# Optimization experiments

Measured on AMD Instinct MI355X. Metric: run time of the kernel, lower is better.

Reference implementation:

```python
import jax, jax.numpy as jnp
from jax import lax
import numpy as np

B, C, HH, WW = 8, 64, 128, 128
N = HH * WW
EPS = 1e-5


def _roll_h(xn, sign):
    # per-channel cyclic roll along H: out[b,c,h,w] = xn[b,c,(h - sign*c) % H, w]
    _, Cx, Hx, _ = xn.shape
    c = jnp.arange(Cx)[:, None]
    idx = (jnp.arange(Hx)[None, :] - sign * jnp.arange(Cx)[:, None]) % Hx  # (C,H)
    return xn[:, c, idx, :]


def _roll_w(xn, sign):
    return _roll_h(xn.transpose(0, 1, 3, 2), sign).transpose(0, 1, 3, 2)


def _ch_linear(xn, w, b):
    # nn.Linear over the channel dim of a BCHW tensor (token-MLP on (B,N,C))
    return jnp.einsum('bchw,cd->bdhw', xn, w) + b[None, :, None, None]


def _bn(xn, g, b):
    # BatchNorm2d, training-mode stats (biased var over B,H,W)
    m = xn.mean(axis=(0, 2, 3), keepdims=True)
    v = xn.var(axis=(0, 2, 3), keepdims=True)
    return (xn - m) * lax.rsqrt(v + EPS) * g[None, :, None, None] + b[None, :, None, None]


def _dwconv(xn, w, dil, pad):
    return lax.conv_general_dilated(xn, w, (1, 1), ((pad, pad), (pad, pad)),
                                    rhs_dilation=(dil, dil),
                                    dimension_numbers=('NCHW', 'OIHW', 'NCHW'),
                                    feature_group_count=xn.shape[1])


def _pc(xn, w):
    # 1x1 pointwise conv, no bias; w: (C_out, C_in)
    return jnp.einsum('bchw,oc->bohw', xn, w)


def lgff_forward(x, fc1_w, fc1_b, fc2_w, fc2_b, fc3_w, fc3_b, fc4_w, fc4_b,
                 fc5_w, fc5_b, ln_g, ln_b, pc_w, dw_w, dw_b, dw_bn_g, dw_bn_b,
                 dd_w, dd_bn_g, dd_bn_b, se_w1, se_b1, se_w2, se_b2, H, W):
    Bx, Nx, Cx = x.shape
    xn = x.transpose(0, 2, 1).reshape(Bx, Cx, H, W)
    # branch 1: roll+c along H -> fc1 -> GELU -> roll+c along W -> fc2
    a = jax.nn.gelu(_ch_linear(_roll_h(xn, 1), fc1_w, fc1_b), approximate=False)
    x_1 = _ch_linear(_roll_w(a, 1), fc2_w, fc2_b) + xn
    # branch 2: roll-c along W -> fc3 -> GELU -> roll+c along H -> fc4
    b = jax.nn.gelu(_ch_linear(_roll_w(xn, -1), fc3_w, fc3_b), approximate=False)
    x_2 = _ch_linear(_roll_h(b, 1), fc4_w, fc4_b) + xn
    # concat along feature dim (token layout dim=2 == channel dim here), LayerNorm(2C), fc5
    xc = jnp.concatenate([x_1, x_2], axis=1)  # (B, 2C, H, W)
    m = xc.mean(axis=1, keepdims=True)
    v = xc.var(axis=1, keepdims=True)
    xc = (xc - m) * lax.rsqrt(v + EPS) * ln_g[None, :, None, None] + ln_b[None, :, None, None]
    x1 = _ch_linear(xc, fc5_w, fc5_b) + xn
    # conv fusion part
    x2 = _pc(x1, pc_w)
    y = jax.nn.relu(_bn(_dwconv(x2, dw_w, 1, 1) + dw_b[None, :, None, None], dw_bn_g, dw_bn_b))
    y = jax.nn.relu(_bn(_dwconv(y, dd_w, 2, 2), dd_bn_g, dd_bn_b))
    y = _pc(y, pc_w)
    # four branches x3..x6 share identical weights/input -> identical outputs
    x7 = 4.0 * (x2 * y)
    # SE block
    s = x7.mean(axis=(2, 3), keepdims=True)  # (B,C,1,1)
    e = jax.nn.relu(jnp.einsum('bcij,oc->boij', s, se_w1) + se_b1[None, :, None, None])
    e = jax.nn.sigmoid(jnp.einsum('bcij,oc->boij', e, se_w2) + se_b2[None, :, None, None])
    return x7 + x7 * e  # (B, C, H, W)


def setup_inputs():
    key = jax.random.key(0)
    ks = jax.random.split(key, 12)
    r = C // 8
    inp = {
        'x': jax.random.normal(ks[0], (B, N, C), jnp.float32),
        'fc1_w': jax.random.normal(ks[1], (C, C), jnp.float32) * 0.02,
        'fc1_b': jnp.zeros((C,), jnp.float32),
        'fc2_w': jax.random.normal(ks[2], (C, C), jnp.float32) * 0.02,
        'fc2_b': jnp.zeros((C,), jnp.float32),
        'fc3_w': jax.random.normal(ks[3], (C, C), jnp.float32) * 0.02,
        'fc3_b': jnp.zeros((C,), jnp.float32),
        'fc4_w': jax.random.normal(ks[4], (C, C), jnp.float32) * 0.02,
        'fc4_b': jnp.zeros((C,), jnp.float32),
        'fc5_w': jax.random.normal(ks[5], (2 * C, C), jnp.float32) * 0.02,
        'fc5_b': jnp.zeros((C,), jnp.float32),
        'ln_g': jnp.ones((2 * C,), jnp.float32),
        'ln_b': jnp.zeros((2 * C,), jnp.float32),
        'pc_w': jax.random.normal(ks[6], (C, C), jnp.float32) * np.sqrt(2.0 / C).astype(np.float32),
        'dw_w': jax.random.normal(ks[7], (C, 1, 3, 3), jnp.float32) * np.sqrt(2.0 / 9.0).astype(np.float32),
        'dw_b': jnp.zeros((C,), jnp.float32),
        'dw_bn_g': jnp.ones((C,), jnp.float32),
        'dw_bn_b': jnp.zeros((C,), jnp.float32),
        'dd_w': jax.random.normal(ks[8], (C, 1, 3, 3), jnp.float32) * np.sqrt(2.0 / 9.0).astype(np.float32),
        'dd_bn_g': jnp.ones((C,), jnp.float32),
        'dd_bn_b': jnp.zeros((C,), jnp.float32),
        'se_w1': jax.random.normal(ks[9], (r, C), jnp.float32) * np.sqrt(2.0 / r).astype(np.float32),
        'se_b1': jnp.zeros((r,), jnp.float32),
        'se_w2': jax.random.normal(ks[10], (C, r), jnp.float32) * np.sqrt(2.0 / C).astype(np.float32),
        'se_b2': jnp.zeros((C,), jnp.float32),
        'H': HH,
        'W': WW,
    }
    return inp


def reference(x, fc1_w, fc1_b, fc2_w, fc2_b, fc3_w, fc3_b, fc4_w, fc4_b,
              fc5_w, fc5_b, ln_g, ln_b, pc_w, dw_w, dw_b, dw_bn_g, dw_bn_b,
              dd_w, dd_bn_g, dd_bn_b, se_w1, se_b1, se_w2, se_b2, H, W):
    return lgff_forward(x, fc1_w, fc1_b, fc2_w, fc2_b, fc3_w, fc3_b, fc4_w, fc4_b,
                        fc5_w, fc5_b, ln_g, ln_b, pc_w, dw_w, dw_b, dw_bn_g, dw_bn_b,
                        dd_w, dd_bn_g, dd_bn_b, se_w1, se_b1, se_w2, se_b2, H, W)
```

## Files before the change

kernel.cpp:

```cpp
#include <hip/hip_runtime.h>

constexpr int NB  = 8;
constexpr int NC  = 64;
constexpr int NH  = 128;
constexpr int NW  = 128;
constexpr int NHW = NH * NW;
constexpr int CHW = NC * NHW;
constexpr int SZ  = NB * CHW;
constexpr int NPOS = NB * NHW;
constexpr float EPS = 1e-5f;

typedef unsigned short u16;
using bf8   = __attribute__((ext_vector_type(8))) short;
using u16x8 = __attribute__((ext_vector_type(8))) u16;
using f32x4 = __attribute__((ext_vector_type(4))) float;

static __device__ inline short f2bf(float f) {
    union { float f; unsigned int u; } v; v.f = f;
    unsigned int r = v.u + 0x7fffu + ((v.u >> 16) & 1u);
    return (short)(r >> 16);
}
static __device__ inline float bf2f(u16 u) {
    union { unsigned int i; float f; } v; v.i = ((unsigned int)u) << 16;
    return v.f;
}

__global__ void k_transpose(const float* __restrict__ x, u16* __restrict__ xn) {
    __shared__ float t[64 * 65];
    int b   = blockIdx.x >> 8;
    int hw0 = (blockIdx.x & 255) << 6;
    int tid = threadIdx.x;
    #pragma unroll
    for (int k = 0; k < 16; ++k) {
        int idx = tid + (k << 8);
        int c = idx & 63, hwl = idx >> 6;
        t[c * 65 + hwl] = x[((size_t)b * NHW + hw0 + hwl) * NC + c];
    }
    __syncthreads();
    #pragma unroll
    for (int k = 0; k < 16; ++k) {
        int idx = tid + (k << 8);
        int hwl = idx & 63, c = idx >> 6;
        xn[(size_t)(b * NC + c) * NHW + hw0 + hwl] = (u16)f2bf(t[c * 65 + hwl]);
    }
}

__global__ void k_pq(const float* __restrict__ w5, const float* __restrict__ lng,
                     const float* __restrict__ lnb, float* __restrict__ PQ) {
    int d = threadIdx.x;
    float P = 0.f, Q = 0.f;
    for (int c = 0; c < 128; ++c) {
        float wv = w5[c * 64 + d];
        P += lng[c] * wv;
        Q += lnb[c] * wv;
    }
    PQ[d] = P; PQ[64 + d] = Q;
}

__global__ __launch_bounds__(256) void
k_mfc2(const u16* __restrict__ xn,
       const float* __restrict__ w1, const float* __restrict__ b1,
       const float* __restrict__ w3, const float* __restrict__ b3,
       u16* __restrict__ t1, u16* __restrict__ t2) {
    __shared__ short wA[64 * 64];
    __shared__ short wB[64 * 64];
    int tid = threadIdx.x;
    int l = tid & 63, wv = tid >> 6;

    #pragma unroll
    for (int i = 0; i < 8; ++i) {
        int c0 = wv * 2 + i * 8;
        unsigned int pa = (unsigned int)(u16)f2bf(w1[c0 * 64 + l]) |
                          ((unsigned int)(u16)f2bf(w1[(c0 + 1) * 64 + l]) << 16);
        *(unsigned int*)&wA[l * 64 + (c0 ^ ((l & 7) << 3))] = pa;
        unsigned int pb = (unsigned int)(u16)f2bf(w3[c0 * 64 + l]) |
                          ((unsigned int)(u16)f2bf(w3[(c0 + 1) * 64 + l]) << 16);
        *(unsigned int*)&wB[l * 64 + (c0 ^ ((l & 7) << 3))] = pb;
    }
    __syncthreads();

    int q = l >> 4, col = l & 15;
    int p  = blockIdx.x * 64 + wv * 16 + col;
    int b  = p >> 14;
    int hw = p & (NHW - 1);
    int h  = hw >> 7, w = hw & 127;
    const u16* inb = xn + (size_t)b * CHW;

    f32x4 acc1[4], acc2[4];
    #pragma unroll
    for (int dt = 0; dt < 4; ++dt) {
        acc1[dt] = (f32x4){0.f, 0.f, 0.f, 0.f};
        acc2[dt] = (f32x4){0.f, 0.f, 0.f, 0.f};
    }
    #pragma unroll
    for (int ks = 0; ks < 2; ++ks) {
        bf8 f1, f2;
        #pragma unroll
        for (int j = 0; j < 8; ++j) {
            int c = ks * 32 + q * 8 + j;
            f1[j] = (short)inb[c * NHW + (((h - c) & 127) << 7) + w];
            f2[j] = (short)inb[c * NHW + (h << 7) + ((w + c) & 127)];
        }
        #pragma unroll
        for (int dt = 0; dt < 4; ++dt) {
            int d = dt * 16 + col;
            int wo = (ks * 32 + q * 8) ^ ((d & 7) << 3);
            acc1[dt] = __builtin_amdgcn_mfma_f32_16x16x32_bf16(*(bf8*)&wA[d * 64 + wo], f1, acc1[dt], 0, 0, 0);
            acc2[dt] = __builtin_amdgcn_mfma_f32_16x16x32_bf16(*(bf8*)&wB[d * 64 + wo], f2, acc2[dt], 0, 0, 0);
        }
    }

    size_t obase = (size_t)b * CHW + hw;
    #pragma unroll
    for (int dt = 0; dt < 4; ++dt) {
        #pragma unroll
        for (int r = 0; r < 4; ++r) {
            int d = dt * 16 + q * 4 + r;
            float v1 = acc1[dt][r] + b1[d];
            v1 = 0.5f * v1 * (1.f + erff(v1 * 0.70710678118654752f));
            float v2 = acc2[dt][r] + b3[d];
            v2 = 0.5f * v2 * (1.f + erff(v2 * 0.70710678118654752f));
            t1[obase + (size_t)d * NHW] = (u16)f2bf(v1);
            t2[obase + (size_t)d * NHW] = (u16)f2bf(v2);
        }
    }
}

__global__ __launch_bounds__(256) void
k_ffuse(const u16* __restrict__ t1, const u16* __restrict__ t2,
        const u16* __restrict__ xnb,
        const float* __restrict__ fc2w, const float* __restrict__ fc2b,
        const float* __restrict__ fc4w, const float* __restrict__ fc4b,
        const float* __restrict__ w5, const float* __restrict__ lng,
        const float* __restrict__ PQ, const float* __restrict__ b5,
        u16* __restrict__ x1out) {
    __shared__ short wA[64 * 64];
    __shared__ short wB[64 * 64];
    __shared__ short wG[64 * 128];
    __shared__ short xt[64 * 136];

    int tid = threadIdx.x;
    int l = tid & 63, wv = tid >> 6;

    #pragma unroll
    for (int i = 0; i < 8; ++i) {
        int c0 = wv * 2 + i * 8;
        unsigned int pa = (unsigned int)(u16)f2bf(fc2w[c0 * 64 + l]) |
                          ((unsigned int)(u16)f2bf(fc2w[(c0 + 1) * 64 + l]) << 16);
        *(unsigned int*)&wA[l * 64 + (c0 ^ ((l & 7) << 3))] = pa;
        unsigned int pb = (unsigned int)(u16)f2bf(fc4w[c0 * 64 + l]) |
                          ((unsigned int)(u16)f2bf(fc4w[(c0 + 1) * 64 + l]) << 16);
        *(unsigned int*)&wB[l * 64 + (c0 ^ ((l & 7) << 3))] = pb;
    }
    #pragma unroll
    for (int i = 0; i < 16; ++i) {
        int c0 = wv * 2 + i * 8;
        unsigned int pk = (unsigned int)(u16)f2bf(lng[c0] * w5[c0 * 64 + l]) |
                          ((unsigned int)(u16)f2bf(lng[c0 + 1] * w5[(c0 + 1) * 64 + l]) << 16);
        *(unsigned int*)&wG[l * 128 + (c0 ^ ((l & 7) << 3))] = pk;
    }
    __syncthreads();

    int q = l >> 4, col = l & 15;
    int p  = blockIdx.x * 64 + wv * 16 + col;
    int b  = p >> 14;
    int hw = p & (NHW - 1);
    int h  = hw >> 7, w = hw & 127;
    size_t base = (size_t)b * CHW;
    int pos = wv * 16 + col;

    f32x4 acc1[4], acc2[4];
    #pragma unroll
    for (int dt = 0; dt < 4; ++dt) {
        acc1[dt] = (f32x4){0.f, 0.f, 0.f, 0.f};
        acc2[dt] = (f32x4){0.f, 0.f, 0.f, 0.f};
    }
    #pragma unroll
    for (int ks = 0; ks < 2; ++ks) {
        bf8 f1, f2;
        #pragma unroll
        for (int j = 0; j < 8; ++j) {
            int c = ks * 32 + q * 8 + j;
            f1[j] = (short)t1[base + c * NHW + (h << 7) + ((w - c) & 127)];
            f2[j] = (short)t2[base + c * NHW + (((h - c) & 127) << 7) + w];
        }
        #pragma unroll
        for (int dt = 0; dt < 4; ++dt) {
            int d = dt * 16 + col;
            int wo = (ks * 32 + q * 8) ^ ((d & 7) << 3);
            acc1[dt] = __builtin_amdgcn_mfma_f32_16x16x32_bf16(*(bf8*)&wA[d * 64 + wo], f1, acc1[dt], 0, 0, 0);
            acc2[dt] = __builtin_amdgcn_mfma_f32_16x16x32_bf16(*(bf8*)&wB[d * 64 + wo], f2, acc2[dt], 0, 0, 0);
        }
    }

    float xr[16];
    #pragma unroll
    for (int dt = 0; dt < 4; ++dt)
        #pragma unroll
        for (int r = 0; r < 4; ++r)
            xr[dt * 4 + r] = bf2f(xnb[base + (size_t)(dt * 16 + q * 4 + r) * NHW + hw]);

    float s = 0.f, sq = 0.f;
    #pragma unroll
    for (int dt = 0; dt < 4; ++dt) {
        float v1[4], v2[4];
        #pragma unroll
        for (int r = 0; r < 4; ++r) {
            int d = dt * 16 + q * 4 + r;
            v1[r] = acc1[dt][r] + fc2b[d] + xr[dt * 4 + r];
            v2[r] = acc2[dt][r] + fc4b[d] + xr[dt * 4 + r];
            s += v1[r] + v2[r];
            sq += v1[r] * v1[r] + v2[r] * v2[r];
        }
        unsigned int pk0 = (unsigned int)(u16)f2bf(v1[0]) | ((unsigned int)(u16)f2bf(v1[1]) << 16);
        unsigned int pk1 = (unsigned int)(u16)f2bf(v1[2]) | ((unsigned int)(u16)f2bf(v1[3]) << 16);
        *(uint2*)&xt[pos * 136 + dt * 16 + q * 4] = make_uint2(pk0, pk1);
        unsigned int pk2 = (unsigned int)(u16)f2bf(v2[0]) | ((unsigned int)(u16)f2bf(v2[1]) << 16);
        unsigned int pk3 = (unsigned int)(u16)f2bf(v2[2]) | ((unsigned int)(u16)f2bf(v2[3]) << 16);
        *(uint2*)&xt[pos * 136 + 64 + dt * 16 + q * 4] = make_uint2(pk2, pk3);
    }
    s  += __shfl_xor(s, 16);  s += __shfl_xor(s, 32);
    sq += __shfl_xor(sq, 16); sq += __shfl_xor(sq, 32);
    float m    = s * (1.f / 128.f);
    float var  = sq * (1.f / 128.f) - m * m;
    float rstd = rsqrtf(var + EPS);
    float mr   = m * rstd;
    __syncthreads();

    f32x4 acc[4];
    #pragma unroll
    for (int dt = 0; dt < 4; ++dt) acc[dt] = (f32x4){0.f, 0.f, 0.f, 0.f};
    #pragma unroll
    for (int ks = 0; ks < 4; ++ks) {
        bf8 bfr = *(bf8*)&xt[pos * 136 + ks * 32 + q * 8];
        #pragma unroll
        for (int dt = 0; dt < 4; ++dt) {
            int d = dt * 16 + col;
            bf8 afr = *(bf8*)&wG[d * 128 + ((ks * 32 + q * 8) ^ ((d & 7) << 3))];
            acc[dt] = __builtin_amdgcn_mfma_f32_16x16x32_bf16(afr, bfr, acc[dt], 0, 0, 0);
        }
    }

    size_t obase = base + hw;
    #pragma unroll
    for (int dt = 0; dt < 4; ++dt) {
        #pragma unroll
        for (int r = 0; r < 4; ++r) {
            int d = dt * 16 + q * 4 + r;
            float val = rstd * acc[dt][r] + PQ[64 + d] - mr * PQ[d] + b5[d] + xr[dt * 4 + r];
            x1out[obase + (size_t)d * NHW] = (u16)f2bf(val);
        }
    }
}

template<bool BNRELU_IN>
__global__ __launch_bounds__(256) void
k_mfc(const u16* __restrict__ in, const float* __restrict__ wgt,
      const float* __restrict__ meanc, const float* __restrict__ rstdc,
      const float* __restrict__ bng, const float* __restrict__ bnb,
      u16* __restrict__ out) {
    __shared__ short wt[64 * 64];
    __shared__ float scl[64], sft[64];
    int tid = threadIdx.x;
    int l = tid & 63, wv = tid >> 6;

    #pragma unroll
    for (int i = 0; i < 16; ++i) {
        int d = wv * 16 + i;
        wt[d * 64 + (l ^ ((d & 7) << 3))] = f2bf(wgt[d * 64 + l]);
    }
    if (BNRELU_IN && tid < 64) {
        float s = rstdc[tid] * bng[tid];
        scl[tid] = s;
        sft[tid] = bnb[tid] - meanc[tid] * s;
    }
    __syncthreads();

    int q = l >> 4, col = l & 15;
    int p  = blockIdx.x * 64 + wv * 16 + col;
    int b  = p >> 14;
    int hw = p & (NHW - 1);
    const u16* inb = in + (size_t)b * CHW;

    f32x4 acc[4];
    #pragma unroll
    for (int dt = 0; dt < 4; ++dt) acc[dt] = (f32x4){0.f, 0.f, 0.f, 0.f};

    #pragma unroll
    for (int ks = 0; ks < 2; ++ks) {
        bf8 bfr;
        #pragma unroll
        for (int j = 0; j < 8; ++j) {
            int c = ks * 32 + q * 8 + j;
            u16 raw = inb[c * NHW + hw];
            if (BNRELU_IN) {
                float v = fmaxf(bf2f(raw) * scl[c] + sft[c], 0.f);
                bfr[j] = f2bf(v);
            } else {
                bfr[j] = (short)raw;
            }
        }
        #pragma unroll
        for (int dt = 0; dt < 4; ++dt) {
            int d = dt * 16 + col;
            bf8 afr = *(bf8*)&wt[d * 64 + ((ks * 32 + q * 8) ^ ((d & 7) << 3))];
            acc[dt] = __builtin_amdgcn_mfma_f32_16x16x32_bf16(afr, bfr, acc[dt], 0, 0, 0);
        }
    }

    size_t obase = (size_t)b * CHW + hw;
    #pragma unroll
    for (int dt = 0; dt < 4; ++dt)
        #pragma unroll
        for (int r = 0; r < 4; ++r) {
            int d = dt * 16 + q * 4 + r;
            out[obase + (size_t)d * NHW] = (u16)f2bf(acc[dt][r]);
        }
}

template<int DIL, bool HASBIAS, bool BNIN>
__global__ __launch_bounds__(256) void
k_dwlds(const u16* __restrict__ in, const float* __restrict__ wgt,
        const float* __restrict__ bias,
        const float* __restrict__ meanc, const float* __restrict__ rstdc,
        const float* __restrict__ bng, const float* __restrict__ bnb,
        u16* __restrict__ out, float* __restrict__ psum, float* __restrict__ psq) {
    constexpr int STR = 136;
    __shared__ float tile[36 * STR];
    __shared__ float ss[256], sq[256];

    int blk = ((blockIdx.x & 7) << 8) | (blockIdx.x >> 3);
    int q   = blk & 3;
    int bc  = blk >> 2;
    int c   = bc & 63;
    int r0  = q * 32;
    int tid = threadIdx.x;
    const u16* ip = in + (size_t)bc * NHW;

    float scale = 0.f, shift = 0.f;
    if (BNIN) { scale = rstdc[c] * bng[c]; shift = bnb[c] - meanc[c] * scale; }

    #pragma unroll 1
    for (int idx = tid; idx < 36 * 16; idx += 256) {
        int lr = idx >> 4, u = idx & 15;
        int gr = r0 - 2 + lr;
        float v[8] = {0.f, 0.f, 0.f, 0.f, 0.f, 0.f, 0.f, 0.f};
        if (gr >= 0 && gr < NH) {
            u16x8 raw = *(const u16x8*)(ip + gr * NW + u * 8);
            #pragma unroll
            for (int j = 0; j < 8; ++j) {
                float f = bf2f(raw[j]);
                if (BNIN) f = fmaxf(f * scale + shift, 0.f);
                v[j] = f;
            }
        }
        *(float4*)&tile[lr * STR + 4 + u * 8]     = make_float4(v[0], v[1], v[2], v[3]);
        *(float4*)&tile[lr * STR + 4 + u * 8 + 4] = make_float4(v[4], v[5], v[6], v[7]);
        if (u == 0)  *(float4*)&tile[lr * STR]       = make_float4(0.f, 0.f, 0.f, 0.f);
        if (u == 15) *(float4*)&tile[lr * STR + 132] = make_float4(0.f, 0.f, 0.f, 0.f);
    }
    __syncthreads();

    float wc[9];
    #pragma unroll
    for (int k = 0; k < 9; ++k) wc[k] = wgt[c * 9 + k];

    int row  = tid >> 3;
    int col0 = (tid & 7) * 16;
    float o[16];
    float bb = HASBIAS ? bias[c] : 0.f;
    #pragma unroll
    for (int j = 0; j < 16; ++j) o[j] = bb;

    #pragma unroll
    for (int i = 0; i < 3; ++i) {
        const float* rp = &tile[(row + 2 + (i - 1) * DIL) * STR + 4 + col0];
        float4 A  = *(const float4*)(rp - 4);
        float4 B0 = *(const float4*)(rp);
        float4 B1 = *(const float4*)(rp + 4);
        float4 B2 = *(const float4*)(rp + 8);
        float4 B3 = *(const float4*)(rp + 12);
        float4 Cc = *(const float4*)(rp + 16);
        float ww[24] = {A.x,A.y,A.z,A.w, B0.x,B0.y,B0.z,B0.w, B1.x,B1.y,B1.z,B1.w,
                        B2.x,B2.y,B2.z,B2.w, B3.x,B3.y,B3.z,B3.w, Cc.x,Cc.y,Cc.z,Cc.w};
        float w0 = wc[3 * i], w1 = wc[3 * i + 1], w2 = wc[3 * i + 2];
        #pragma unroll
        for (int j = 0; j < 16; ++j)
            o[j] += w0 * ww[4 + j - DIL] + w1 * ww[4 + j] + w2 * ww[4 + j + DIL];
    }

    u16* op = out + (size_t)bc * NHW + (r0 + row) * NW + col0;
    u16x8 o1, o2;
    #pragma unroll
    for (int j = 0; j < 8; ++j) { o1[j] = (u16)f2bf(o[j]); o2[j] = (u16)f2bf(o[8 + j]); }
    *(u16x8*)(op)     = o1;
    *(u16x8*)(op + 8) = o2;

    float s = 0.f, qq = 0.f;
    #pragma unroll
    for (int j = 0; j < 16; ++j) { s += o[j]; qq += o[j] * o[j]; }
    ss[tid] = s; sq[tid] = qq; __syncthreads();
    for (int off = 128; off > 0; off >>= 1) {
        if (tid < off) { ss[tid] += ss[tid + off]; sq[tid] += sq[tid + off]; }
        __syncthreads();
    }
    if (tid == 0) { psum[blk] = ss[0]; psq[blk] = sq[0]; }
}

__global__ void k_bn_finalize(const float* __restrict__ psum, const float* __restrict__ psq,
                              float* __restrict__ meanc, float* __restrict__ rstdc) {
    int c = threadIdx.x;
    float s = 0.f, qv = 0.f;
    for (int b = 0; b < NB; ++b)
        #pragma unroll
        for (int j = 0; j < 4; ++j) {
            int idx = ((b * 64 + c) << 2) + j;
            s += psum[idx]; qv += psq[idx];
        }
    const float inv = 1.f / (float)(NB * NHW);
    float m = s * inv;
    float v = qv * inv - m * m;
    meanc[c] = m;
    rstdc[c] = rsqrtf(v + EPS);
}

__global__ void k_se_reduce(const u16* __restrict__ x2, const u16* __restrict__ y3,
                            float* __restrict__ s4) {
    __shared__ float ss[256];
    int q   = blockIdx.x & 3;
    int bc  = blockIdx.x >> 2;
    int tid = threadIdx.x;
    const u16* a  = x2 + (size_t)bc * NHW + q * (NHW / 4);
    const u16* b_ = y3 + (size_t)bc * NHW + q * (NHW / 4);
    float acc = 0.f;
    #pragma unroll
    for (int i = 0; i < 2; ++i) {
        u16x8 av = *(const u16x8*)(a + (tid + i * 256) * 8);
        u16x8 bv = *(const u16x8*)(b_ + (tid + i * 256) * 8);
        #pragma unroll
        for (int j = 0; j < 8; ++j) acc += bf2f(av[j]) * bf2f(bv[j]);
    }
    ss[tid] = acc; __syncthreads();
    for (int o = 128; o > 0; o >>= 1) {
        if (tid < o) ss[tid] += ss[tid + o];
        __syncthreads();
    }
    if (tid == 0) s4[blockIdx.x] = ss[0];
}

__global__ void k_se_mlp(const float* __restrict__ s4, const float* __restrict__ w1,
                         const float* __restrict__ b1, const float* __restrict__ w2,
                         const float* __restrict__ b2, float* __restrict__ e) {
    __shared__ float sh[64], e1[8];
    int b = blockIdx.x, tid = threadIdx.x;
    float sv = 0.f;
    #pragma unroll
    for (int j = 0; j < 4; ++j) sv += s4[(b * 64 + tid) * 4 + j];
    sh[tid] = sv * (4.f / (float)NHW);
    __syncthreads();
    if (tid < 8) {
        float a = b1[tid];
        for (int c = 0; c < 64; ++c) a += sh[c] * w1[tid * 64 + c];
        e1[tid] = a > 0.f ? a : 0.f;
    }
    __syncthreads();
    float a = b2[tid];
    #pragma unroll
    for (int j = 0; j < 8; ++j) a += e1[j] * w2[tid * 8 + j];
    e[b * 64 + tid] = 1.f / (1.f + expf(-a));
}

__global__ void k_final8(const u16* __restrict__ x2, const u16* __restrict__ y3,
                         const float* __restrict__ e, float* __restrict__ out) {
    int t  = blockIdx.x * 256 + threadIdx.x;
    int bc = t >> 11;
    float f = 4.f * (1.f + e[bc]);
    u16x8 av = *(const u16x8*)(x2 + (size_t)t * 8);
    u16x8 bv = *(const u16x8*)(y3 + (size_t)t * 8);
    float4 o0, o1;
    o0.x = f * bf2f(av[0]) * bf2f(bv[0]); o0.y = f * bf2f(av[1]) * bf2f(bv[1]);
    o0.z = f * bf2f(av[2]) * bf2f(bv[2]); o0.w = f * bf2f(av[3]) * bf2f(bv[3]);
    o1.x = f * bf2f(av[4]) * bf2f(bv[4]); o1.y = f * bf2f(av[5]) * bf2f(bv[5]);
    o1.z = f * bf2f(av[6]) * bf2f(bv[6]); o1.w = f * bf2f(av[7]) * bf2f(bv[7]);
    *(float4*)(out + (size_t)t * 8)     = o0;
    *(float4*)(out + (size_t)t * 8 + 4) = o1;
}

extern "C" void kernel_launch(void* const* d_in, const int* in_sizes, int n_in,
                              void* d_out, int out_size, void* d_ws, size_t ws_size,
                              hipStream_t stream) {
    const float* x     = (const float*)d_in[0];
    const float* fc1w  = (const float*)d_in[1];
    const float* fc1b  = (const float*)d_in[2];
    const float* fc2w  = (const float*)d_in[3];
    const float* fc2b  = (const float*)d_in[4];
    const float* fc3w  = (const float*)d_in[5];
    const float* fc3b  = (const float*)d_in[6];
    const float* fc4w  = (const float*)d_in[7];
    const float* fc4b  = (const float*)d_in[8];
    const float* fc5w  = (const float*)d_in[9];
    const float* fc5b  = (const float*)d_in[10];
    const float* lng   = (const float*)d_in[11];
    const float* lnb   = (const float*)d_in[12];
    const float* pcw   = (const float*)d_in[13];
    const float* dww   = (const float*)d_in[14];
    const float* dwb   = (const float*)d_in[15];
    const float* dwbng = (const float*)d_in[16];
    const float* dwbnb = (const float*)d_in[17];
    const float* ddw   = (const float*)d_in[18];
    const float* ddbng = (const float*)d_in[19];
    const float* ddbnb = (const float*)d_in[20];
    const float* sew1  = (const float*)d_in[21];
    const float* seb1  = (const float*)d_in[22];
    const float* sew2  = (const float*)d_in[23];
    const float* seb2  = (const float*)d_in[24];

    float* out = (float*)d_out;
    u16* wsu = (u16*)d_ws;
    u16* bufA = wsu;
    u16* bufB = wsu + (size_t)SZ;
    u16* bufC = wsu + (size_t)2 * SZ;
    u16* bufD = wsu + (size_t)3 * SZ;
    float* st = (float*)(wsu + (size_t)4 * SZ);
    float* psumA  = st;
    float* psqA   = st + 2048;
    float* meanc1 = st + 4096;
    float* rstdc1 = st + 4160;
    float* meanc2 = st + 4224;
    float* rstdc2 = st + 4288;
    float* svec   = st + 4352;
    float* evec   = st + 6400;
    float* pqv    = st + 6912;

    dim3 blk(256);
    const float* nil = nullptr;

    k_transpose<<<NB * (NHW / 64), blk, 0, stream>>>(x, bufA);
    k_pq<<<1, 64, 0, stream>>>(fc5w, lng, lnb, pqv);
    k_mfc2<<<NPOS / 64, blk, 0, stream>>>(bufA, fc1w, fc1b, fc3w, fc3b, bufB, bufC);
    k_ffuse<<<NPOS / 64, blk, 0, stream>>>(bufB, bufC, bufA, fc2w, fc2b, fc4w, fc4b,
                                           fc5w, lng, pqv, fc5b, bufD);
    k_mfc<false><<<NPOS / 64, blk, 0, stream>>>(bufD, pcw, nil, nil, nil, nil, bufA);
    k_dwlds<1, true, false><<<2048, blk, 0, stream>>>(bufA, dww, dwb, nil, nil, nil, nil, bufB, psumA, psqA);
    k_bn_finalize<<<1, 64, 0, stream>>>(psumA, psqA, meanc1, rstdc1);
    k_dwlds<2, false, true><<<2048, blk, 0, stream>>>(bufB, ddw, nil, meanc1, rstdc1, dwbng, dwbnb, bufC, psumA, psqA);
    k_bn_finalize<<<1, 64, 0, stream>>>(psumA, psqA, meanc2, rstdc2);
    k_mfc<true><<<NPOS / 64, blk, 0, stream>>>(bufC, pcw, meanc2, rstdc2, ddbng, ddbnb, bufD);
    k_se_reduce<<<NB * NC * 4, blk, 0, stream>>>(bufA, bufD, svec);
    k_se_mlp<<<NB, 64, 0, stream>>>(svec, sew1, seb1, sew2, seb2, evec);
    k_final8<<<SZ / 2048, blk, 0, stream>>>(bufA, bufD, evec, out);
}
```

Measured before the change: 153.4 us.

## Stage rolled inputs in LDS and fold BN-finalize and SE-MLP into consumer kernels

```diff
diff --git a/kernel.cpp b/kernel.cpp
--- a/kernel.cpp
+++ b/kernel.cpp
@@ -58,14 +58,22 @@
 }
 
 __global__ __launch_bounds__(256) void
-k_mfc2(const u16* __restrict__ xn,
-       const float* __restrict__ w1, const float* __restrict__ b1,
-       const float* __restrict__ w3, const float* __restrict__ b3,
-       u16* __restrict__ t1, u16* __restrict__ t2) {
+k_mfc2s(const u16* __restrict__ xn,
+        const float* __restrict__ w1, const float* __restrict__ b1,
+        const float* __restrict__ w3, const float* __restrict__ b3,
+        u16* __restrict__ t1, u16* __restrict__ t2) {
     __shared__ short wA[64 * 64];
     __shared__ short wB[64 * 64];
+    __shared__ u16 tA[64 * 68];
+    __shared__ u16 tB[64 * 132];
     int tid = threadIdx.x;
     int l = tid & 63, wv = tid >> 6;
+
+    int p0 = blockIdx.x * 64;
+    int b  = p0 >> 14;
+    int hw0 = p0 & (NHW - 1);
+    int h  = hw0 >> 7, w0 = hw0 & 127;
+    const u16* inb = xn + (size_t)b * CHW;
 
     #pragma unroll
     for (int i = 0; i < 8; ++i) {
@@ -77,14 +85,23 @@
                           ((unsigned int)(u16)f2bf(w3[(c0 + 1) * 64 + l]) << 16);
         *(unsigned int*)&wB[l * 64 + (c0 ^ ((l & 7) << 3))] = pb;
     }
+    #pragma unroll
+    for (int k = 0; k < 2; ++k) {
+        int i = tid + k * 256;
+        int c = i >> 3, seg = i & 7;
+        int gr = (h - c) & 127;
+        *(u16x8*)&tA[c * 68 + seg * 8] = *(const u16x8*)(inb + c * NHW + gr * NW + w0 + seg * 8);
+    }
+    #pragma unroll
+    for (int k = 0; k < 4; ++k) {
+        int i = tid + k * 256;
+        int c = i >> 4, seg = i & 15;
+        *(u16x8*)&tB[c * 132 + seg * 8] = *(const u16x8*)(inb + c * NHW + h * NW + seg * 8);
+    }
     __syncthreads();
 
     int q = l >> 4, col = l & 15;
-    int p  = blockIdx.x * 64 + wv * 16 + col;
-    int b  = p >> 14;
-    int hw = p & (NHW - 1);
-    int h  = hw >> 7, w = hw & 127;
-    const u16* inb = xn + (size_t)b * CHW;
+    int pidx = wv * 16 + col;
 
     f32x4 acc1[4], acc2[4];
     #pragma unroll
@@ -98,8 +115,8 @@
         #pragma unroll
         for (int j = 0; j < 8; ++j) {
             int c = ks * 32 + q * 8 + j;
-            f1[j] = (short)inb[c * NHW + (((h - c) & 127) << 7) + w];
-            f2[j] = (short)inb[c * NHW + (h << 7) + ((w + c) & 127)];
+            f1[j] = (short)tA[c * 68 + pidx];
+            f2[j] = (short)tB[c * 132 + ((w0 + pidx + c) & 127)];
         }
         #pragma unroll
         for (int dt = 0; dt < 4; ++dt) {
@@ -110,7 +127,7 @@
         }
     }
 
-    size_t obase = (size_t)b * CHW + hw;
+    size_t obase = (size_t)b * CHW + hw0;
     #pragma unroll
     for (int dt = 0; dt < 4; ++dt) {
         #pragma unroll
@@ -120,8 +137,8 @@
             v1 = 0.5f * v1 * (1.f + erff(v1 * 0.70710678118654752f));
             float v2 = acc2[dt][r] + b3[d];
             v2 = 0.5f * v2 * (1.f + erff(v2 * 0.70710678118654752f));
-            t1[obase + (size_t)d * NHW] = (u16)f2bf(v1);
-            t2[obase + (size_t)d * NHW] = (u16)f2bf(v2);
+            t1[obase + (size_t)d * NHW + pidx - pidx + ((wv * 16 + col))] = (u16)f2bf(v1);
+            t2[obase + (size_t)d * NHW + ((wv * 16 + col))] = (u16)f2bf(v2);
         }
     }
 }
@@ -256,7 +273,7 @@
 template<bool BNRELU_IN>
 __global__ __launch_bounds__(256) void
 k_mfc(const u16* __restrict__ in, const float* __restrict__ wgt,
-      const float* __restrict__ meanc, const float* __restrict__ rstdc,
+      const float* __restrict__ psum, const float* __restrict__ psq,
       const float* __restrict__ bng, const float* __restrict__ bnb,
       u16* __restrict__ out) {
     __shared__ short wt[64 * 64];
@@ -270,9 +287,20 @@
         wt[d * 64 + (l ^ ((d & 7) << 3))] = f2bf(wgt[d * 64 + l]);
     }
     if (BNRELU_IN && tid < 64) {
-        float s = rstdc[tid] * bng[tid];
-        scl[tid] = s;
-        sft[tid] = bnb[tid] - meanc[tid] * s;
+        float s = 0.f, qv = 0.f;
+        #pragma unroll
+        for (int i = 0; i < 32; ++i) {
+            int bb = i >> 2, j = i & 3;
+            int idx = ((bb * 64 + tid) << 2) + j;
+            s += psum[idx]; qv += psq[idx];
+        }
+        const float inv = 1.f / (float)(NB * NHW);
+        float m = s * inv;
+        float var = qv * inv - m * m;
+        float rs = rsqrtf(var + EPS);
+        float sc = rs * bng[tid];
+        scl[tid] = sc;
+        sft[tid] = bnb[tid] - m * sc;
     }
     __syncthreads();
 
@@ -322,9 +350,9 @@
 __global__ __launch_bounds__(256) void
 k_dwlds(const u16* __restrict__ in, const float* __restrict__ wgt,
         const float* __restrict__ bias,
-        const float* __restrict__ meanc, const float* __restrict__ rstdc,
+        const float* __restrict__ psumIn, const float* __restrict__ psqIn,
         const float* __restrict__ bng, const float* __restrict__ bnb,
-        u16* __restrict__ out, float* __restrict__ psum, float* __restrict__ psq) {
+        u16* __restrict__ out, float* __restrict__ psumOut, float* __restrict__ psqOut) {
     constexpr int STR = 136;
     __shared__ float tile[36 * STR];
     __shared__ float ss[256], sq[256];
@@ -338,7 +366,21 @@
     const u16* ip = in + (size_t)bc * NHW;
 
     float scale = 0.f, shift = 0.f;
-    if (BNIN) { scale = rstdc[c] * bng[c]; shift = bnb[c] - meanc[c] * scale; }
+    if (BNIN) {
+        float s = 0.f, qv = 0.f;
+        #pragma unroll
+        for (int i = 0; i < 32; ++i) {
+            int bb = i >> 2, j = i & 3;
+            int idx = ((bb * 64 + c) << 2) + j;
+            s += psumIn[idx]; qv += psqIn[idx];
+        }
+        const float inv = 1.f / (float)(NB * NHW);
+        float m = s * inv;
+        float var = qv * inv - m * m;
+        float rs = rsqrtf(var + EPS);
+        scale = rs * bng[c];
+        shift = bnb[c] - m * scale;
+    }
 
     #pragma unroll 1
     for (int idx = tid; idx < 36 * 16; idx += 256) {
@@ -404,24 +446,7 @@
         if (tid < off) { ss[tid] += ss[tid + off]; sq[tid] += sq[tid + off]; }
         __syncthreads();
     }
-    if (tid == 0) { psum[blk] = ss[0]; psq[blk] = sq[0]; }
-}
-
-__global__ void k_bn_finalize(const float* __restrict__ psum, const float* __restrict__ psq,
-                              float* __restrict__ meanc, float* __restrict__ rstdc) {
-    int c = threadIdx.x;
-    float s = 0.f, qv = 0.f;
-    for (int b = 0; b < NB; ++b)
-        #pragma unroll
-        for (int j = 0; j < 4; ++j) {
-            int idx = ((b * 64 + c) << 2) + j;
-            s += psum[idx]; qv += psq[idx];
-        }
-    const float inv = 1.f / (float)(NB * NHW);
-    float m = s * inv;
-    float v = qv * inv - m * m;
-    meanc[c] = m;
-    rstdc[c] = rsqrtf(v + EPS);
+    if (tid == 0) { psumOut[blk] = ss[0]; psqOut[blk] = sq[0]; }
 }
 
 __global__ void k_se_reduce(const u16* __restrict__ x2, const u16* __restrict__ y3,
@@ -448,33 +473,39 @@
     if (tid == 0) s4[blockIdx.x] = ss[0];
 }
 
-__global__ void k_se_mlp(const float* __restrict__ s4, const float* __restrict__ w1,
-                         const float* __restrict__ b1, const float* __restrict__ w2,
-                         const float* __restrict__ b2, float* __restrict__ e) {
-    __shared__ float sh[64], e1[8];
-    int b = blockIdx.x, tid = threadIdx.x;
-    float sv = 0.f;
-    #pragma unroll
-    for (int j = 0; j < 4; ++j) sv += s4[(b * 64 + tid) * 4 + j];
-    sh[tid] = sv * (4.f / (float)NHW);
+__global__ void k_final8(const u16* __restrict__ x2, const u16* __restrict__ y3,
+                         const float* __restrict__ s4,
+                         const float* __restrict__ w1, const float* __restrict__ b1,
+                         const float* __restrict__ w2, const float* __restrict__ b2,
+                         float* __restrict__ out) {
+    __shared__ float sh[64], e1[8], ev[1];
+    int tid = threadIdx.x;
+    int bc = blockIdx.x >> 3;
+    int b  = bc >> 6, c = bc & 63;
+
+    if (tid < 64) {
+        float sv = 0.f;
+        #pragma unroll
+        for (int j = 0; j < 4; ++j) sv += s4[(b * 64 + tid) * 4 + j];
+        sh[tid] = sv * (4.f / (float)NHW);
+    }
     __syncthreads();
     if (tid < 8) {
         float a = b1[tid];
-        for (int c = 0; c < 64; ++c) a += sh[c] * w1[tid * 64 + c];
+        for (int cc = 0; cc < 64; ++cc) a += sh[cc] * w1[tid * 64 + cc];
         e1[tid] = a > 0.f ? a : 0.f;
     }
     __syncthreads();
-    float a = b2[tid];
-    #pragma unroll
-    for (int j = 0; j < 8; ++j) a += e1[j] * w2[tid * 8 + j];
-    e[b * 64 + tid] = 1.f / (1.f + expf(-a));
-}
-
-__global__ void k_final8(const u16* __restrict__ x2, const u16* __restrict__ y3,
-                         const float* __restrict__ e, float* __restrict__ out) {
-    int t  = blockIdx.x * 256 + threadIdx.x;
-    int bc = t >> 11;
-    float f = 4.f * (1.f + e[bc]);
+    if (tid == 0) {
+        float a = b2[c];
+        #pragma unroll
+        for (int j = 0; j < 8; ++j) a += e1[j] * w2[c * 8 + j];
+        ev[0] = 1.f / (1.f + expf(-a));
+    }
+    __syncthreads();
+
+    int t = blockIdx.x * 256 + tid;
+    float f = 4.f * (1.f + ev[0]);
     u16x8 av = *(const u16x8*)(x2 + (size_t)t * 8);
     u16x8 bv = *(const u16x8*)(y3 + (size_t)t * 8);
     float4 o0, o1;
@@ -522,31 +553,25 @@
     u16* bufC = wsu + (size_t)2 * SZ;
     u16* bufD = wsu + (size_t)3 * SZ;
     float* st = (float*)(wsu + (size_t)4 * SZ);
-    float* psumA  = st;
-    float* psqA   = st + 2048;
-    float* meanc1 = st + 4096;
-    float* rstdc1 = st + 4160;
-    float* meanc2 = st + 4224;
-    float* rstdc2 = st + 4288;
-    float* svec   = st + 4352;
-    float* evec   = st + 6400;
-    float* pqv    = st + 6912;
+    float* psumA = st;
+    float* psqA  = st + 2048;
+    float* psumB = st + 4096;
+    float* psqB  = st + 6144;
+    float* svec  = st + 8192;
+    float* pqv   = st + 10240;
 
     dim3 blk(256);
     const float* nil = nullptr;
 
     k_transpose<<<NB * (NHW / 64), blk, 0, stream>>>(x, bufA);
     k_pq<<<1, 64, 0, stream>>>(fc5w, lng, lnb, pqv);
-    k_mfc2<<<NPOS / 64, blk, 0, stream>>>(bufA, fc1w, fc1b, fc3w, fc3b, bufB, bufC);
+    k_mfc2s<<<NPOS / 64, blk, 0, stream>>>(bufA, fc1w, fc1b, fc3w, fc3b, bufB, bufC);
     k_ffuse<<<NPOS / 64, blk, 0, stream>>>(bufB, bufC, bufA, fc2w, fc2b, fc4w, fc4b,
                                            fc5w, lng, pqv, fc5b, bufD);
     k_mfc<false><<<NPOS / 64, blk, 0, stream>>>(bufD, pcw, nil, nil, nil, nil, bufA);
     k_dwlds<1, true, false><<<2048, blk, 0, stream>>>(bufA, dww, dwb, nil, nil, nil, nil, bufB, psumA, psqA);
-    k_bn_finalize<<<1, 64, 0, stream>>>(psumA, psqA, meanc1, rstdc1);
-    k_dwlds<2, false, true><<<2048, blk, 0, stream>>>(bufB, ddw, nil, meanc1, rstdc1, dwbng, dwbnb, bufC, psumA, psqA);
-    k_bn_finalize<<<1, 64, 0, stream>>>(psumA, psqA, meanc2, rstdc2);
-    k_mfc<true><<<NPOS / 64, blk, 0, stream>>>(bufC, pcw, meanc2, rstdc2, ddbng, ddbnb, bufD);
+    k_dwlds<2, false, true><<<2048, blk, 0, stream>>>(bufB, ddw, nil, psumA, psqA, dwbng, dwbnb, bufC, psumB, psqB);
+    k_mfc<true><<<NPOS / 64, blk, 0, stream>>>(bufC, pcw, psumB, psqB, ddbng, ddbnb, bufD);
     k_se_reduce<<<NB * NC * 4, blk, 0, stream>>>(bufA, bufD, svec);
-    k_se_mlp<<<NB, 64, 0, stream>>>(svec, sew1, seb1, sew2, seb2, evec);
-    k_final8<<<SZ / 2048, blk, 0, stream>>>(bufA, bufD, evec, out);
-}
+    k_final8<<<SZ / 2048, blk, 0, stream>>>(bufA, bufD, svec, sew1, seb1, sew2, seb2, out);
+}
```

Result: no change. 154.3 us (+0.5%).
